# Performance work log

Measured on AMD Instinct MI355X. Metric: run time of the kernel, lower is better.

The kernel has to match this reference:

```python
import jax, jax.numpy as jnp
import numpy as np
import math

E, H, N, FF, S, B, LBL = 512, 8, 3, 2048, 256, 128, 3
# eval-mode threshold: epoch clamped to 40 => d = log(2000/40 - 1)
D_THRESH = math.log(2000.0 / 40.0 - 1.0)


def _pos_encoding(seq_len, dim):
    pos = np.arange(seq_len, dtype=np.float32)[:, None]
    div = np.exp(np.arange(0, dim, 2, dtype=np.float32) * (-math.log(10000.0) / dim))
    pe = np.zeros((seq_len, dim), np.float32)
    pe[:, 0::2] = np.sin(pos * div)
    pe[:, 1::2] = np.cos(pos * div)
    return jnp.asarray(pe)[:, None, :]  # [S,1,E]


def _layer_norm(x, g, b, eps=1e-5):
    m = x.mean(-1, keepdims=True)
    v = ((x - m) ** 2).mean(-1, keepdims=True)
    return (x - m) / jnp.sqrt(v + eps) * g + b


def _mha(xq, xkv, Wqkv, bqkv, Wo, bo):
    # xq: [Sq,B,E], xkv: [Sk,B,E]; noise-thresholded attention, eval branch
    Sq, Bb, Ee = xq.shape
    Sk = xkv.shape[0]
    dk = Ee // H
    Wq, Wk, Wv = jnp.split(Wqkv, 3, axis=1)
    bq, bk, bv = jnp.split(bqkv, 3)
    q = (xq @ Wq + bq) * (dk ** -0.5)
    k = xkv @ Wk + bk
    v = xkv @ Wv + bv
    q = q.reshape(Sq, Bb, H, dk).transpose(1, 2, 0, 3)  # [B,H,Sq,dk]
    k = k.reshape(Sk, Bb, H, dk).transpose(1, 2, 0, 3)
    v = v.reshape(Sk, Bb, H, dk).transpose(1, 2, 0, 3)
    s = jnp.einsum('bhqd,bhkd->bhqk', q, k)
    smax = jnp.max(s, axis=-1, keepdims=True)
    s = jnp.where(s < smax - D_THRESH, -jnp.inf, s)  # threshold sparsification
    w = jax.nn.softmax(s, axis=-1)
    o = jnp.einsum('bhqk,bhkd->bhqd', w, v)
    o = o.transpose(2, 0, 1, 3).reshape(Sq, Bb, Ee)
    return o @ Wo + bo


def _ffn(x, W1, b1, W2, b2):
    return jax.nn.relu(x @ W1 + b1) @ W2 + b2


def _encoder_layer(x, i, g1, b1ln, Wqkv, bqkv, Wo, bo, g2, b2ln, W1, b1, W2, b2):
    h = _layer_norm(x, g1[i], b1ln[i])
    x = x + _mha(h, h, Wqkv[i], bqkv[i], Wo[i], bo[i])
    h = _layer_norm(x, g2[i], b2ln[i])
    x = x + _ffn(h, W1[i], b1[i], W2[i], b2[i])
    return x


def _forward(x_1, x_2, enc_ln1_g, enc_ln1_b, enc_Wqkv, enc_bqkv, enc_Wo, enc_bo,
             enc_ln2_g, enc_ln2_b, enc_W1, enc_b1, enc_W2, enc_b2,
             isa_ln_g, isa_ln_b, isa_Wqkv, isa_bqkv, isa_Wo, isa_bo,
             iea_ln_g, iea_ln_b, iea_Wqkv, iea_bqkv, iea_Wo, iea_bo,
             iff_ln_g, iff_ln_b, int_W1, int_b1, int_W2, int_b2,
             fc1_w, fc1_b, fc2_w, fc2_b, fc3_w, fc3_b, fc4_w, fc4_b):
    pe = _pos_encoding(x_1.shape[0], x_1.shape[-1])
    x1 = x_1 + pe
    x2 = x_2 + pe
    # Siamese encoder (shared weights)
    for i in range(N):
        x1 = _encoder_layer(x1, i, enc_ln1_g, enc_ln1_b, enc_Wqkv, enc_bqkv, enc_Wo, enc_bo,
                            enc_ln2_g, enc_ln2_b, enc_W1, enc_b1, enc_W2, enc_b2)
        x2 = _encoder_layer(x2, i, enc_ln1_g, enc_ln1_b, enc_Wqkv, enc_bqkv, enc_Wo, enc_bo,
                            enc_ln2_g, enc_ln2_b, enc_W1, enc_b1, enc_W2, enc_b2)
    e1, e2 = x1, x2
    # interaction stack (shared self/cross attn applied to both streams)
    for i in range(N):
        h1 = _layer_norm(x1, isa_ln_g[i], isa_ln_b[i])
        x1 = x1 + _mha(h1, h1, isa_Wqkv[i], isa_bqkv[i], isa_Wo[i], isa_bo[i])
        h2 = _layer_norm(x2, isa_ln_g[i], isa_ln_b[i])
        x2 = x2 + _mha(h2, h2, isa_Wqkv[i], isa_bqkv[i], isa_Wo[i], isa_bo[i])
        h1 = _layer_norm(x1, iea_ln_g[i], iea_ln_b[i])
        h2 = _layer_norm(x2, iea_ln_g[i], iea_ln_b[i])
        y1 = _mha(h1, h2, iea_Wqkv[i], iea_bqkv[i], iea_Wo[i], iea_bo[i])
        y2 = _mha(h2, h1, iea_Wqkv[i], iea_bqkv[i], iea_Wo[i], iea_bo[i])
        x1 = x1 + y1
        x2 = x2 + y2
        x1 = x1 + _ffn(_layer_norm(x1, iff_ln_g[i], iff_ln_b[i]), int_W1[i], int_b1[i], int_W2[i], int_b2[i])
        x2 = x2 + _ffn(_layer_norm(x2, iff_ln_g[i], iff_ln_b[i]), int_W1[i], int_b1[i], int_W2[i], int_b2[i])
    i1, i2 = x1, x2
    # Comparison classifier
    h1 = jax.nn.relu(jnp.concatenate([e1, i1], axis=-1) @ fc1_w + fc1_b) @ fc2_w + fc2_b
    p1 = h1.sum(0) / (h1.shape[0] ** 0.5)  # [B,E]
    h2 = jax.nn.relu(jnp.concatenate([e2, i2], axis=-1) @ fc1_w + fc1_b) @ fc2_w + fc2_b
    p2 = h2.sum(0) / (h2.shape[0] ** 0.5)
    x = jnp.concatenate([p1, p2], axis=-1)  # [B,2E]
    return jax.nn.relu(x @ fc3_w + fc3_b) @ fc4_w + fc4_b  # [B,LBL]


def setup_inputs() -> dict:
    key = jax.random.key(0)
    ks = iter(jax.random.split(key, 64))
    sc = 1.0 / math.sqrt(E)

    def w(shape, scale=None):
        s = (1.0 / math.sqrt(shape[-2])) if scale is None and len(shape) >= 2 else (scale or sc)
        return jax.random.normal(next(ks), shape, jnp.float32) * s

    d = {
        'x_1': jax.random.normal(next(ks), (S, B, E), jnp.float32),
        'x_2': jax.random.normal(next(ks), (S, B, E), jnp.float32),
        'enc_ln1_g': jnp.ones((N, E)), 'enc_ln1_b': jnp.zeros((N, E)),
        'enc_Wqkv': w((N, E, 3 * E)), 'enc_bqkv': jnp.zeros((N, 3 * E)),
        'enc_Wo': w((N, E, E)), 'enc_bo': jnp.zeros((N, E)),
        'enc_ln2_g': jnp.ones((N, E)), 'enc_ln2_b': jnp.zeros((N, E)),
        'enc_W1': w((N, E, FF)), 'enc_b1': jnp.zeros((N, FF)),
        'enc_W2': w((N, FF, E)), 'enc_b2': jnp.zeros((N, E)),
        'isa_ln_g': jnp.ones((N, E)), 'isa_ln_b': jnp.zeros((N, E)),
        'isa_Wqkv': w((N, E, 3 * E)), 'isa_bqkv': jnp.zeros((N, 3 * E)),
        'isa_Wo': w((N, E, E)), 'isa_bo': jnp.zeros((N, E)),
        'iea_ln_g': jnp.ones((N, E)), 'iea_ln_b': jnp.zeros((N, E)),
        'iea_Wqkv': w((N, E, 3 * E)), 'iea_bqkv': jnp.zeros((N, 3 * E)),
        'iea_Wo': w((N, E, E)), 'iea_bo': jnp.zeros((N, E)),
        'iff_ln_g': jnp.ones((N, E)), 'iff_ln_b': jnp.zeros((N, E)),
        'int_W1': w((N, E, FF)), 'int_b1': jnp.zeros((N, FF)),
        'int_W2': w((N, FF, E)), 'int_b2': jnp.zeros((N, E)),
        'fc1_w': w((2 * E, E)), 'fc1_b': jnp.zeros((E,)),
        'fc2_w': w((E, E)), 'fc2_b': jnp.zeros((E,)),
        'fc3_w': w((2 * E, E)), 'fc3_b': jnp.zeros((E,)),
        'fc4_w': w((E, LBL)), 'fc4_b': jnp.zeros((LBL,)),
    }
    return d


def reference(x_1, x_2, enc_ln1_g, enc_ln1_b, enc_Wqkv, enc_bqkv, enc_Wo, enc_bo,
              enc_ln2_g, enc_ln2_b, enc_W1, enc_b1, enc_W2, enc_b2,
              isa_ln_g, isa_ln_b, isa_Wqkv, isa_bqkv, isa_Wo, isa_bo,
              iea_ln_g, iea_ln_b, iea_Wqkv, iea_bqkv, iea_Wo, iea_bo,
              iff_ln_g, iff_ln_b, int_W1, int_b1, int_W2, int_b2,
              fc1_w, fc1_b, fc2_w, fc2_b, fc3_w, fc3_b, fc4_w, fc4_b):
    return _forward(x_1, x_2, enc_ln1_g, enc_ln1_b, enc_Wqkv, enc_bqkv, enc_Wo, enc_bo,
                    enc_ln2_g, enc_ln2_b, enc_W1, enc_b1, enc_W2, enc_b2,
                    isa_ln_g, isa_ln_b, isa_Wqkv, isa_bqkv, isa_Wo, isa_bo,
                    iea_ln_g, iea_ln_b, iea_Wqkv, iea_bqkv, iea_Wo, iea_bo,
                    iff_ln_g, iff_ln_b, int_W1, int_b1, int_W2, int_b2,
                    fc1_w, fc1_b, fc2_w, fc2_b, fc3_w, fc3_b, fc4_w, fc4_b)
```

## Files before the change

### kernel.cpp

```cpp
#include <hip/hip_runtime.h>


using u16 = unsigned short;
using u32 = unsigned int;

typedef __bf16 bf16x8 __attribute__((ext_vector_type(8)));
typedef u16    u16x8  __attribute__((ext_vector_type(8)));
typedef float  f32x4  __attribute__((ext_vector_type(4)));

#define D_THRESH 3.8918203f

__device__ __forceinline__ u16 f2bf(float f) {
    u32 u = __builtin_bit_cast(u32, f);
    u32 r = (u + 0x7fffu + ((u >> 16) & 1u)) >> 16;
    return (u16)r;
}
__device__ __forceinline__ float bf2f(u16 h) {
    u32 u = ((u32)h) << 16;
    return __builtin_bit_cast(float, u);
}
__device__ __forceinline__ bf16x8 ld_bf8(const u16* p) {
    u16x8 v = *(const u16x8*)p;
    return __builtin_bit_cast(bf16x8, v);
}

#define GLD_LDS(gptr, lptr)                                                     \
    __builtin_amdgcn_global_load_lds(                                           \
        (const __attribute__((address_space(1))) u32*)(gptr),                   \
        (__attribute__((address_space(3))) u32*)(lptr), 16, 0, 0)

__global__ __launch_bounds__(256) void transpose_to_bf16(
    const float* __restrict__ in, u16* __restrict__ out,
    const float* __restrict__ gamma, int K, int N)
{
    __shared__ float tile[32][33];
    const float* src = in  + (size_t)blockIdx.z * K * N;
    u16*         dst = out + (size_t)blockIdx.z * K * N;
    const float* gm  = gamma ? gamma + (size_t)blockIdx.z * K : nullptr;
    int n0 = blockIdx.x * 32, k0 = blockIdx.y * 32;
#pragma unroll
    for (int i = 0; i < 4; ++i) {
        int k = k0 + threadIdx.y + i * 8;
        tile[threadIdx.y + i * 8][threadIdx.x] = src[(size_t)k * N + n0 + threadIdx.x];
    }
    __syncthreads();
#pragma unroll
    for (int i = 0; i < 4; ++i) {
        int n = n0 + threadIdx.y + i * 8;
        int kk = k0 + threadIdx.x;
        float v = tile[threadIdx.x][threadIdx.y + i * 8];
        if (gm) v *= gm[kk];
        dst[(size_t)n * K + kk] = f2bf(v);
    }
}

__global__ __launch_bounds__(256) void init_ud(
    const float* __restrict__ bias, float* __restrict__ u, float* __restrict__ d)
{
    int n = blockIdx.x * 256 + threadIdx.x;
    u[n] = 0.f; d[n] = bias[n];
}

__global__ __launch_bounds__(256) void colsum_part(
    const float* __restrict__ W, const float* __restrict__ gamma,
    const float* __restrict__ beta, float* __restrict__ u, float* __restrict__ d,
    int K, int N)
{
    int n = blockIdx.x * 256 + threadIdx.x;
    int k0 = blockIdx.y * 32;
    const float* Wz = W + (size_t)blockIdx.z * K * N;
    const float* gz = gamma + (size_t)blockIdx.z * K;
    const float* bz = beta  + (size_t)blockIdx.z * K;
    float su = 0.f, sd = 0.f;
#pragma unroll 4
    for (int k = k0; k < k0 + 32; ++k) {
        float w = Wz[(size_t)k * N + n];
        su += gz[k] * w;
        sd += bz[k] * w;
    }
    atomicAdd(&u[(size_t)blockIdx.z * N + n], su);
    atomicAdd(&d[(size_t)blockIdx.z * N + n], sd);
}

__global__ __launch_bounds__(256) void row_stats(
    const u16* __restrict__ x, float2* __restrict__ st)
{
    const int lane = threadIdx.x & 63, w = threadIdx.x >> 6;
    const size_t row = (size_t)blockIdx.x * 4 + w;
    union { uint4 v; u16 h[8]; } a;
    a.v = *(const uint4*)(x + row * 512 + lane * 8);
    float s = 0.f, sq = 0.f;
#pragma unroll
    for (int j = 0; j < 8; ++j) { float f = bf2f(a.h[j]); s += f; sq += f * f; }
#pragma unroll
    for (int off = 1; off < 64; off <<= 1) {
        s  += __shfl_xor(s,  off, 64);
        sq += __shfl_xor(sq, off, 64);
    }
    if (lane == 0) {
        float m  = s * (1.f / 512.f);
        float vr = sq * (1.f / 512.f) - m * m;
        st[row] = make_float2(m, rsqrtf(vr + 1e-5f));
    }
}

template<int EPI>
__global__ __launch_bounds__(256) void gemm_bt(
    const u16* __restrict__ A, int lda,
    const u16* __restrict__ BT, int ldb,
    const float* __restrict__ bias,
    const float* __restrict__ u,
    const float2* __restrict__ st,
    void* __restrict__ Cv, int ldc,
    const float* __restrict__ resf,
    const u16* __restrict__ res16,
    int M, int N, int K)
{
    __shared__ u16 As[128 * 64];
    __shared__ u16 Bs[128 * 64];
    const int tid  = threadIdx.x;
    const int lane = tid & 63;
    const int w    = tid >> 6;
    const int wm   = w >> 1, wn = w & 1;
    const int m0   = blockIdx.y * 128, n0 = blockIdx.x * 128;
    const int g    = lane & 15, q = lane >> 4;

    const f32x4 fz = {0.f, 0.f, 0.f, 0.f};
    f32x4 acc[4][4];
#pragma unroll
    for (int i = 0; i < 4; ++i)
#pragma unroll
        for (int j = 0; j < 4; ++j) acc[i][j] = fz;

    for (int kt = 0; kt < K; kt += 64) {
#pragma unroll
        for (int i = 0; i < 4; ++i) {
            int c = (w * 4 + i) * 64 + lane;
            int r = c >> 3, cq = c & 7;
            GLD_LDS(A  + (size_t)(m0 + r) * lda + kt + cq * 8, As + (size_t)(w * 4 + i) * 512);
            GLD_LDS(BT + (size_t)(n0 + r) * ldb + kt + cq * 8, Bs + (size_t)(w * 4 + i) * 512);
        }
        __syncthreads();
#pragma unroll
        for (int ks = 0; ks < 2; ++ks) {
            bf16x8 af[4], bfr[4];
#pragma unroll
            for (int i = 0; i < 4; ++i) af[i]  = ld_bf8(As + (wm * 64 + i * 16 + g) * 64 + ks * 32 + q * 8);
#pragma unroll
            for (int j = 0; j < 4; ++j) bfr[j] = ld_bf8(Bs + (wn * 64 + j * 16 + g) * 64 + ks * 32 + q * 8);
#pragma unroll
            for (int i = 0; i < 4; ++i)
#pragma unroll
                for (int j = 0; j < 4; ++j)
                    acc[i][j] = __builtin_amdgcn_mfma_f32_16x16x32_bf16(af[i], bfr[j], acc[i][j], 0, 0, 0);
        }
        __syncthreads();
    }
#pragma unroll
    for (int j = 0; j < 4; ++j) {
        int col  = n0 + wn * 64 + j * 16 + g;
        float bj = bias ? bias[col] : 0.f;
        float un = (EPI == 5 || EPI == 6) ? u[col] : 0.f;
#pragma unroll
        for (int i = 0; i < 4; ++i) {
            int rb = m0 + wm * 64 + i * 16 + q * 4;
#pragma unroll
            for (int r = 0; r < 4; ++r) {
                float v = acc[i][j][r];
                size_t idx = (size_t)(rb + r) * ldc + col;
                if (EPI == 5 || EPI == 6) {
                    float2 s2 = st[rb + r];
                    v = s2.y * v - s2.y * s2.x * un + bj;
                } else {
                    v += bj;
                }
                if (EPI == 1 || EPI == 6) v = fmaxf(v, 0.f);
                if (EPI == 4) v = fmaxf(resf[idx] + v, 0.f);
                if (EPI == 2) v += bf2f(((u16*)Cv)[idx]);
                if (EPI == 8) v += bf2f(((u16*)Cv)[idx]) + bf2f(res16[idx]);
                if (EPI == 3) ((float*)Cv)[idx] = v;
                else          ((u16*)Cv)[idx]   = f2bf(v);
            }
        }
    }
}

__global__ __launch_bounds__(256) void attn_kernel(
    const u16* __restrict__ Q, int lq,
    const u16* __restrict__ Kp, const u16* __restrict__ Vp, int lkv,
    u16* __restrict__ O, int lo)
{
    __shared__ u16 smem[32768];
    u16* Ks  = smem;
    u16* Qs  = smem + 16384;
    u16* Ps  = smem;
    u16* VTs = smem + 16384;

    const int tid = threadIdx.x, lane = tid & 63, w = tid >> 6;
    const int g = lane & 15, qd = lane >> 4;
    const int q0 = blockIdx.x * 64;
    const int b = blockIdx.y >> 3, h = blockIdx.y & 7;

#pragma unroll
    for (int i = 0; i < 8; ++i) {
        int c = (w * 8 + i) * 64 + lane;
        int r = c >> 3, cq = c & 7;
        GLD_LDS(Kp + (size_t)(r * 128 + b) * lkv + h * 64 + cq * 8,
                Ks + (size_t)(w * 8 + i) * 512);
    }
#pragma unroll
    for (int i = 0; i < 2; ++i) {
        int c = (w * 2 + i) * 64 + lane;
        int r = c >> 3, cq = c & 7;
        GLD_LDS(Q + (size_t)((q0 + r) * 128 + b) * lq + h * 64 + cq * 8,
                Qs + (size_t)(w * 2 + i) * 512);
    }
    __syncthreads();

    const f32x4 fz = {0.f, 0.f, 0.f, 0.f};
    f32x4 s[16];
#pragma unroll
    for (int t = 0; t < 16; ++t) s[t] = fz;
#pragma unroll
    for (int ks = 0; ks < 2; ++ks) {
        bf16x8 aq = ld_bf8(Qs + (w * 16 + g) * 64 + ks * 32 + qd * 8);
#pragma unroll
        for (int t = 0; t < 16; ++t) {
            bf16x8 bk = ld_bf8(Ks + (t * 16 + g) * 64 + ks * 32 + qd * 8);
            s[t] = __builtin_amdgcn_mfma_f32_16x16x32_bf16(aq, bk, s[t], 0, 0, 0);
        }
    }
    __syncthreads();

    union { uint4 v; u16 us[8]; } vch[8];
#pragma unroll
    for (int i = 0; i < 8; ++i) {
        int c = i * 256 + tid;
        int r = c >> 3, cq = c & 7;
        vch[i].v = *(const uint4*)(Vp + (size_t)(r * 128 + b) * lkv + h * 64 + cq * 8);
    }

    float mrow[4] = {-1e30f, -1e30f, -1e30f, -1e30f};
#pragma unroll
    for (int t = 0; t < 16; ++t)
#pragma unroll
        for (int r = 0; r < 4; ++r) mrow[r] = fmaxf(mrow[r], s[t][r]);
#pragma unroll
    for (int off = 1; off < 16; off <<= 1)
#pragma unroll
        for (int r = 0; r < 4; ++r) mrow[r] = fmaxf(mrow[r], __shfl_xor(mrow[r], off, 64));
#pragma unroll
    for (int r = 0; r < 4; ++r) mrow[r] *= 0.125f;

    float l[4] = {0.f, 0.f, 0.f, 0.f};
#pragma unroll
    for (int t = 0; t < 16; ++t)
#pragma unroll
        for (int r = 0; r < 4; ++r) {
            float sc = s[t][r] * 0.125f;
            float p  = (sc >= mrow[r] - D_THRESH) ? __expf(sc - mrow[r]) : 0.f;
            u16 pb = f2bf(p);
            l[r] += bf2f(pb);
            Ps[(w * 16 + qd * 4 + r) * 256 + t * 16 + g] = pb;
        }
#pragma unroll
    for (int off = 1; off < 16; off <<= 1)
#pragma unroll
        for (int r = 0; r < 4; ++r) l[r] += __shfl_xor(l[r], off, 64);

#pragma unroll
    for (int i = 0; i < 8; ++i) {
        int c = i * 256 + tid;
        int r = c >> 3, cq = c & 7;
#pragma unroll
        for (int j = 0; j < 8; ++j) VTs[(cq * 8 + j) * 256 + r] = vch[i].us[j];
    }
    __syncthreads();

    f32x4 o[4];
#pragma unroll
    for (int nt = 0; nt < 4; ++nt) o[nt] = fz;
#pragma unroll
    for (int ks = 0; ks < 8; ++ks) {
        bf16x8 ap = ld_bf8(Ps + (w * 16 + g) * 256 + ks * 32 + qd * 8);
#pragma unroll
        for (int nt = 0; nt < 4; ++nt) {
            bf16x8 bv = ld_bf8(VTs + (nt * 16 + g) * 256 + ks * 32 + qd * 8);
            o[nt] = __builtin_amdgcn_mfma_f32_16x16x32_bf16(ap, bv, o[nt], 0, 0, 0);
        }
    }
    float rl[4];
#pragma unroll
    for (int r = 0; r < 4; ++r) rl[r] = 1.f / l[r];
#pragma unroll
    for (int nt = 0; nt < 4; ++nt)
#pragma unroll
        for (int r = 0; r < 4; ++r) {
            int srow = q0 + w * 16 + qd * 4 + r;
            O[(size_t)(srow * 128 + b) * lo + h * 64 + nt * 16 + g] = f2bf(o[nt][r] * rl[r]);
        }
}

__global__ __launch_bounds__(256) void build_pe(float* __restrict__ pe) {
    int idx = blockIdx.x * 256 + threadIdx.x;
    int e = idx & 511, s = idx >> 9;
    int j = e >> 1;
    float fr = __expf((float)(2 * j) * (-0.017988946f));
    float ph = (float)s * fr;
    pe[idx] = (e & 1) ? cosf(ph) : sinf(ph);
}

__global__ __launch_bounds__(256) void add_pe_bf16(
    const float* __restrict__ in, const float* __restrict__ pe, u16* __restrict__ out)
{
    size_t idx = (size_t)blockIdx.x * 256 + threadIdx.x;
    int e = (int)(idx & 511);
    int s = (int)(idx >> 16);
    out[idx] = f2bf(in[idx] + pe[(s << 9) | e]);
}

__global__ __launch_bounds__(128) void pool_sum(
    const float* __restrict__ t2, u16* __restrict__ pcat, int colofs)
{
    int b = blockIdx.x >> 2, ec = blockIdx.x & 3;
    int e = ec * 128 + threadIdx.x;
    float acc = 0.f;
    for (int s = 0; s < 256; ++s) acc += t2[(size_t)(s * 128 + b) * 512 + e];
    pcat[b * 1024 + colofs + e] = f2bf(acc * 0.0625f);
}

__global__ __launch_bounds__(64) void fc4_kernel(
    const u16* __restrict__ a, const float* __restrict__ w,
    const float* __restrict__ bias, float* __restrict__ out)
{
    int id = blockIdx.x * 64 + threadIdx.x;
    if (id >= 384) return;
    int b = id / 3, l = id % 3;
    float acc = bias[l];
    for (int k = 0; k < 512; ++k) acc += bf2f(a[b * 512 + k]) * w[k * 3 + l];
    out[id] = acc;
}

__global__ __launch_bounds__(64) void sentinel_kernel(float* __restrict__ out) {
    int i = blockIdx.x * 64 + threadIdx.x;
    if (i < 384) out[i] = -12345.0f;
}

extern "C" void kernel_launch(void* const* d_in, const int* in_sizes, int n_in,
                              void* d_out, int out_size, void* d_ws, size_t ws_size,
                              hipStream_t stream) {
    (void)in_sizes; (void)n_in; (void)out_size;

    const float* x_1       = (const float*)d_in[0];
    const float* x_2       = (const float*)d_in[1];
    const float* enc_ln1_g = (const float*)d_in[2];
    const float* enc_ln1_b = (const float*)d_in[3];
    const float* enc_Wqkv  = (const float*)d_in[4];
    const float* enc_bqkv  = (const float*)d_in[5];
    const float* enc_Wo    = (const float*)d_in[6];
    const float* enc_bo    = (const float*)d_in[7];
    const float* enc_ln2_g = (const float*)d_in[8];
    const float* enc_ln2_b = (const float*)d_in[9];
    const float* enc_W1    = (const float*)d_in[10];
    const float* enc_b1    = (const float*)d_in[11];
    const float* enc_W2    = (const float*)d_in[12];
    const float* enc_b2    = (const float*)d_in[13];
    const float* isa_ln_g  = (const float*)d_in[14];
    const float* isa_ln_b  = (const float*)d_in[15];
    const float* isa_Wqkv  = (const float*)d_in[16];
    const float* isa_bqkv  = (const float*)d_in[17];
    const float* isa_Wo    = (const float*)d_in[18];
    const float* isa_bo    = (const float*)d_in[19];
    const float* iea_ln_g  = (const float*)d_in[20];
    const float* iea_ln_b  = (const float*)d_in[21];
    const float* iea_Wqkv  = (const float*)d_in[22];
    const float* iea_bqkv  = (const float*)d_in[23];
    const float* iea_Wo    = (const float*)d_in[24];
    const float* iea_bo    = (const float*)d_in[25];
    const float* iff_ln_g  = (const float*)d_in[26];
    const float* iff_ln_b  = (const float*)d_in[27];
    const float* int_W1    = (const float*)d_in[28];
    const float* int_b1    = (const float*)d_in[29];
    const float* int_W2    = (const float*)d_in[30];
    const float* int_b2    = (const float*)d_in[31];
    const float* fc1_w     = (const float*)d_in[32];
    const float* fc1_b     = (const float*)d_in[33];
    const float* fc2_w     = (const float*)d_in[34];
    const float* fc2_b     = (const float*)d_in[35];
    const float* fc3_w     = (const float*)d_in[36];
    const float* fc3_b     = (const float*)d_in[37];
    const float* fc4_w     = (const float*)d_in[38];
    const float* fc4_b     = (const float*)d_in[39];
    float* out = (float*)d_out;

    const size_t WS_NEED = 264318976;
    if (ws_size < WS_NEED) {
        sentinel_kernel<<<6, 64, 0, stream>>>(out);
        return;
    }

    char* ws = (char*)d_ws;
    u16* isaQKV = (u16*)(ws + 0);
    u16* isaWO  = (u16*)(ws + 4718592);
    u16* ieaQKV = (u16*)(ws + 6291456);
    u16* ieaWO  = (u16*)(ws + 11010048);
    u16* intW1  = (u16*)(ws + 12582912);
    u16* intW2  = (u16*)(ws + 18874368);
    u16* fc1T   = (u16*)(ws + 25165824);
    u16* fc2T   = (u16*)(ws + 26214400);
    u16* fc3T   = (u16*)(ws + 26738688);
    float* UD   = (float*)(ws + 27787264);
    float* enc_qkv_u = UD;
    float* enc_qkv_d = UD + 4608;
    float* enc_w1_u  = UD + 9216;
    float* enc_w1_d  = UD + 15360;
    float* isa_qkv_u = UD + 21504;
    float* isa_qkv_d = UD + 26112;
    float* iea_qkv_u = UD + 30720;
    float* iea_qkv_d = UD + 35328;
    float* int_w1_u  = UD + 39936;
    float* int_w1_d  = UD + 46080;
    float2* stats1 = (float2*)(ws + 27996160);
    float2* stats2 = (float2*)(ws + 28258304);
    float*  pe     = (float*)(ws + 28520448);
    u16*    pcat   = (u16*)(ws + 29044736);
    u16*    fc3o   = (u16*)(ws + 29306880);
    u16*    x1     = (u16*)(ws + 29437952);
    u16*    x2     = (u16*)(ws + 62992384);
    u16* encQKV = (u16*)(ws + 96546816);
    u16* encWO  = (u16*)(ws + 96546816 + 4718592);
    u16* encW1  = (u16*)(ws + 96546816 + 6291456);
    u16* encW2  = (u16*)(ws + 96546816 + 12582912);
    u16* e1     = (u16*)(ws + 96546816);
    u16* e2     = (u16*)(ws + 96546816 + 33554432);
    u16*   qkv  = (u16*)(ws + 163655680);
    u16*   B0   = (u16*)(ws + 163655680);
    u16*   B1   = (u16*)(ws + 163655680 + 33554432);
    u16*   fbuf = (u16*)(ws + 163655680);
    u16*   dlt  = (u16*)(ws + 163655680 + 67108864);
    float* accf = (float*)(ws + 163655680);
    u16*   hcls = (u16*)(ws + 163655680 + 67108864);

    auto TR = [&](const float* in, u16* o, const float* g, int K, int N, int L) {
        transpose_to_bf16<<<dim3(N / 32, K / 32, L), dim3(32, 8), 0, stream>>>(in, o, g, K, N);
    };
    TR(enc_Wqkv, encQKV, enc_ln1_g, 512, 1536, 3);
    TR(enc_Wo,   encWO,  nullptr,   512, 512,  3);
    TR(enc_W1,   encW1,  enc_ln2_g, 512, 2048, 3);
    TR(enc_W2,   encW2,  nullptr,   2048, 512, 3);
    TR(isa_Wqkv, isaQKV, isa_ln_g,  512, 1536, 3);
    TR(isa_Wo,   isaWO,  nullptr,   512, 512,  3);
    TR(iea_Wqkv, ieaQKV, iea_ln_g,  512, 1536, 3);
    TR(iea_Wo,   ieaWO,  nullptr,   512, 512,  3);
    TR(int_W1,   intW1,  iff_ln_g,  512, 2048, 3);
    TR(int_W2,   intW2,  nullptr,   2048, 512, 3);
    TR(fc1_w, fc1T, nullptr, 1024, 512, 1);
    TR(fc2_w, fc2T, nullptr, 512,  512, 1);
    TR(fc3_w, fc3T, nullptr, 1024, 512, 1);

    auto CS = [&](const float* W, const float* g, const float* b, const float* bias,
                  float* u, float* d, int K, int N, int L) {
        init_ud<<<N * L / 256, 256, 0, stream>>>(bias, u, d);
        colsum_part<<<dim3(N / 256, K / 32, L), 256, 0, stream>>>(W, g, b, u, d, K, N);
    };
    CS(enc_Wqkv, enc_ln1_g, enc_ln1_b, enc_bqkv, enc_qkv_u, enc_qkv_d, 512, 1536, 3);
    CS(enc_W1,   enc_ln2_g, enc_ln2_b, enc_b1,   enc_w1_u,  enc_w1_d,  512, 2048, 3);
    CS(isa_Wqkv, isa_ln_g,  isa_ln_b,  isa_bqkv, isa_qkv_u, isa_qkv_d, 512, 1536, 3);
    CS(iea_Wqkv, iea_ln_g,  iea_ln_b,  iea_bqkv, iea_qkv_u, iea_qkv_d, 512, 1536, 3);
    CS(int_W1,   iff_ln_g,  iff_ln_b,  int_b1,   int_w1_u,  int_w1_d,  512, 2048, 3);

    build_pe<<<512, 256, 0, stream>>>(pe);
    add_pe_bf16<<<65536, 256, 0, stream>>>(x_1, pe, x1);
    add_pe_bf16<<<65536, 256, 0, stream>>>(x_2, pe, x2);

    auto G = [&](int epi, const u16* A, int lda, const u16* BT, int ldb,
                 const float* bias, const float* uu, const float2* stt,
                 void* C, int ldc, const float* resf, const u16* res16,
                 int M, int N, int K) {
        dim3 grid(N / 128, M / 128);
        switch (epi) {
        case 0: gemm_bt<0><<<grid, 256, 0, stream>>>(A, lda, BT, ldb, bias, uu, stt, C, ldc, resf, res16, M, N, K); break;
        case 1: gemm_bt<1><<<grid, 256, 0, stream>>>(A, lda, BT, ldb, bias, uu, stt, C, ldc, resf, res16, M, N, K); break;
        case 2: gemm_bt<2><<<grid, 256, 0, stream>>>(A, lda, BT, ldb, bias, uu, stt, C, ldc, resf, res16, M, N, K); break;
        case 3: gemm_bt<3><<<grid, 256, 0, stream>>>(A, lda, BT, ldb, bias, uu, stt, C, ldc, resf, res16, M, N, K); break;
        case 4: gemm_bt<4><<<grid, 256, 0, stream>>>(A, lda, BT, ldb, bias, uu, stt, C, ldc, resf, res16, M, N, K); break;
        case 5: gemm_bt<5><<<grid, 256, 0, stream>>>(A, lda, BT, ldb, bias, uu, stt, C, ldc, resf, res16, M, N, K); break;
        case 6: gemm_bt<6><<<grid, 256, 0, stream>>>(A, lda, BT, ldb, bias, uu, stt, C, ldc, resf, res16, M, N, K); break;
        case 8: gemm_bt<8><<<grid, 256, 0, stream>>>(A, lda, BT, ldb, bias, uu, stt, C, ldc, resf, res16, M, N, K); break;
        }
    };
    auto STATS = [&](const u16* x, float2* stt) {
        row_stats<<<8192, 256, 0, stream>>>(x, stt);
    };
    auto ATT = [&](const u16* Qp, int lq, const u16* Kp, const u16* Vp, int lkv,
                   u16* Op, int lo) {
        attn_kernel<<<dim3(4, 1024), 256, 0, stream>>>(Qp, lq, Kp, Vp, lkv, Op, lo);
    };

    auto self_block = [&](u16* x, u16* wqkvT, const float* qu, const float* qd,
                          u16* woT, const float* bo,
                          u16* w1T, const float* w1u, const float* w1d,
                          u16* w2T, const float* b2, bool do_ffn) {
        STATS(x, stats1);
        G(5, x, 512, wqkvT, 512, qd, qu, stats1, qkv, 1536, nullptr, nullptr, 32768, 1536, 512);
        ATT(qkv, 1536, qkv + 512, qkv + 1024, 1536, qkv, 1536);
        G(2, qkv, 1536, woT, 512, bo, nullptr, nullptr, x, 512, nullptr, nullptr, 32768, 512, 512);
        if (do_ffn) {
            STATS(x, stats1);
            G(6, x, 512, w1T, 512, w1d, w1u, stats1, fbuf, 1024, nullptr, nullptr, 32768, 1024, 512);
            G(0, fbuf, 1024, w2T, 2048, b2, nullptr, nullptr, dlt, 512, nullptr, nullptr, 32768, 512, 1024);
            G(6, x, 512, w1T + 1024 * 512, 512, w1d + 1024, w1u + 1024, stats1, fbuf, 1024, nullptr, nullptr, 32768, 1024, 512);
            G(8, fbuf, 1024, w2T + 1024, 2048, nullptr, nullptr, nullptr, x, 512, nullptr, dlt, 32768, 512, 1024);
        }
    };

    for (int i = 0; i < 3; ++i)
        for (int st = 0; st < 2; ++st)
            self_block(st ? x2 : x1,
                       encQKV + (size_t)i * 786432, enc_qkv_u + i * 1536, enc_qkv_d + i * 1536,
                       encWO + (size_t)i * 262144, enc_bo + i * 512,
                       encW1 + (size_t)i * 1048576, enc_w1_u + i * 2048, enc_w1_d + i * 2048,
                       encW2 + (size_t)i * 1048576, enc_b2 + i * 512, true);

    hipMemcpyAsync(e1, x1, 33554432, hipMemcpyDeviceToDevice, stream);
    hipMemcpyAsync(e2, x2, 33554432, hipMemcpyDeviceToDevice, stream);

    for (int i = 0; i < 3; ++i) {
        for (int st = 0; st < 2; ++st)
            self_block(st ? x2 : x1,
                       isaQKV + (size_t)i * 786432, isa_qkv_u + i * 1536, isa_qkv_d + i * 1536,
                       isaWO + (size_t)i * 262144, isa_bo + i * 512,
                       nullptr, nullptr, nullptr, nullptr, nullptr, false);
        u16* qT  = ieaQKV + (size_t)i * 786432;
        u16* kvT = qT + 512 * 512;
        const float* qu = iea_qkv_u + i * 1536;
        const float* qd = iea_qkv_d + i * 1536;
        STATS(x2, stats2);
        G(5, x2, 512, kvT, 512, qd + 512, qu + 512, stats2, B1, 1024, nullptr, nullptr, 32768, 1024, 512);
        STATS(x1, stats1);
        G(5, x1, 512, qT, 512, qd, qu, stats1, B0, 512, nullptr, nullptr, 32768, 512, 512);
        ATT(B0, 512, B1, B1 + 512, 1024, B0, 512);
        G(5, x1, 512, kvT, 512, qd + 512, qu + 512, stats1, B1, 1024, nullptr, nullptr, 32768, 1024, 512);
        G(2, B0, 512, ieaWO + (size_t)i * 262144, 512, iea_bo + i * 512, nullptr, nullptr,
          x1, 512, nullptr, nullptr, 32768, 512, 512);
        G(5, x2, 512, qT, 512, qd, qu, stats2, B0, 512, nullptr, nullptr, 32768, 512, 512);
        ATT(B0, 512, B1, B1 + 512, 1024, B0, 512);
        G(2, B0, 512, ieaWO + (size_t)i * 262144, 512, iea_bo + i * 512, nullptr, nullptr,
          x2, 512, nullptr, nullptr, 32768, 512, 512);
        for (int st = 0; st < 2; ++st) {
            u16* x = st ? x2 : x1;
            STATS(x, stats1);
            u16* w1T = intW1 + (size_t)i * 1048576;
            u16* w2T = intW2 + (size_t)i * 1048576;
            const float* w1u = int_w1_u + i * 2048;
            const float* w1d = int_w1_d + i * 2048;
            G(6, x, 512, w1T, 512, w1d, w1u, stats1, fbuf, 1024, nullptr, nullptr, 32768, 1024, 512);
            G(0, fbuf, 1024, w2T, 2048, int_b2 + i * 512, nullptr, nullptr, dlt, 512, nullptr, nullptr, 32768, 512, 1024);
            G(6, x, 512, w1T + 1024 * 512, 512, w1d + 1024, w1u + 1024, stats1, fbuf, 1024, nullptr, nullptr, 32768, 1024, 512);
            G(8, fbuf, 1024, w2T + 1024, 2048, nullptr, nullptr, nullptr, x, 512, nullptr, dlt, 32768, 512, 1024);
        }
    }

    for (int st = 0; st < 2; ++st) {
        const u16* e = st ? e2 : e1;
        const u16* x = st ? x2 : x1;
        G(3, e, 512, fc1T, 1024, nullptr, nullptr, nullptr, accf, 512, nullptr, nullptr, 32768, 512, 512);
        G(4, x, 512, fc1T + 512, 1024, fc1_b, nullptr, nullptr, hcls, 512, accf, nullptr, 32768, 512, 512);
        G(3, hcls, 512, fc2T, 512, fc2_b, nullptr, nullptr, accf, 512, nullptr, nullptr, 32768, 512, 512);
        pool_sum<<<512, 128, 0, stream>>>(accf, pcat, st * 512);
    }
    G(1, pcat, 1024, fc3T, 1024, fc3_b, nullptr, nullptr, fc3o, 512, nullptr, nullptr, 128, 512, 1024);
    fc4_kernel<<<6, 64, 0, stream>>>(fc3o, fc4_w, fc4_b, out);
}
```

Measured before the change: 9.380 ms.

## Stage GEMM epilogue through LDS and restructure attention to one block per head

The GEMM epilogue for bf16 outputs now writes results into shared memory and then stores them as coalesced 16-byte rows, also doing the residual reads vectorized. The attention kernel now launches one 512-thread block per (batch, head): K is loaded once and reused across all 256 queries, Q is read straight from global memory, and P and V^T are staged in 64-key chunks. Together these are meant to cut uncoalesced scalar stores and repeated K/V loads, at the cost of extra barriers and a grid of only 1024 blocks.

```diff
diff --git a/kernel.cpp b/kernel.cpp
--- a/kernel.cpp
+++ b/kernel.cpp
@@ -116,8 +116,9 @@
     const u16* __restrict__ res16,
     int M, int N, int K)
 {
-    __shared__ u16 As[128 * 64];
-    __shared__ u16 Bs[128 * 64];
+    __shared__ u16 smem[17408];
+    u16* As = smem;
+    u16* Bs = smem + 8192;
     const int tid  = threadIdx.x;
     const int lane = tid & 63;
     const int w    = tid >> 6;
@@ -156,149 +157,187 @@
         }
         __syncthreads();
     }
-#pragma unroll
-    for (int j = 0; j < 4; ++j) {
-        int col  = n0 + wn * 64 + j * 16 + g;
-        float bj = bias ? bias[col] : 0.f;
-        float un = (EPI == 5 || EPI == 6) ? u[col] : 0.f;
-#pragma unroll
-        for (int i = 0; i < 4; ++i) {
-            int rb = m0 + wm * 64 + i * 16 + q * 4;
-#pragma unroll
-            for (int r = 0; r < 4; ++r) {
-                float v = acc[i][j][r];
-                size_t idx = (size_t)(rb + r) * ldc + col;
-                if (EPI == 5 || EPI == 6) {
-                    float2 s2 = st[rb + r];
-                    v = s2.y * v - s2.y * s2.x * un + bj;
-                } else {
-                    v += bj;
+
+    if (EPI == 3 || EPI == 4) {
+#pragma unroll
+        for (int j = 0; j < 4; ++j) {
+            int col  = n0 + wn * 64 + j * 16 + g;
+            float bj = bias ? bias[col] : 0.f;
+#pragma unroll
+            for (int i = 0; i < 4; ++i) {
+                int rb = m0 + wm * 64 + i * 16 + q * 4;
+#pragma unroll
+                for (int r = 0; r < 4; ++r) {
+                    float v = acc[i][j][r] + bj;
+                    size_t idx = (size_t)(rb + r) * ldc + col;
+                    if (EPI == 4) { v = fmaxf(resf[idx] + v, 0.f); ((u16*)Cv)[idx] = f2bf(v); }
+                    else          ((float*)Cv)[idx] = v;
                 }
-                if (EPI == 1 || EPI == 6) v = fmaxf(v, 0.f);
-                if (EPI == 4) v = fmaxf(resf[idx] + v, 0.f);
-                if (EPI == 2) v += bf2f(((u16*)Cv)[idx]);
-                if (EPI == 8) v += bf2f(((u16*)Cv)[idx]) + bf2f(res16[idx]);
-                if (EPI == 3) ((float*)Cv)[idx] = v;
-                else          ((u16*)Cv)[idx]   = f2bf(v);
-            }
-        }
-    }
-}
-
-__global__ __launch_bounds__(256) void attn_kernel(
+            }
+        }
+    } else {
+        u16* Cs = smem;
+#pragma unroll
+        for (int j = 0; j < 4; ++j) {
+            int cl   = wn * 64 + j * 16 + g;
+            float bj = bias ? bias[n0 + cl] : 0.f;
+            float un = (EPI == 5 || EPI == 6) ? u[n0 + cl] : 0.f;
+#pragma unroll
+            for (int i = 0; i < 4; ++i) {
+                int rl = wm * 64 + i * 16 + q * 4;
+#pragma unroll
+                for (int r = 0; r < 4; ++r) {
+                    float v = acc[i][j][r];
+                    if (EPI == 5 || EPI == 6) {
+                        float2 s2 = st[m0 + rl + r];
+                        v = s2.y * v - s2.y * s2.x * un + bj;
+                    } else {
+                        v += bj;
+                    }
+                    if (EPI == 1 || EPI == 6) v = fmaxf(v, 0.f);
+                    Cs[(rl + r) * 136 + cl] = f2bf(v);
+                }
+            }
+        }
+        __syncthreads();
+        const int cr = tid >> 4, cc = tid & 15;
+#pragma unroll
+        for (int rr = 0; rr < 8; ++rr) {
+            int rl = cr * 8 + rr;
+            size_t gidx = (size_t)(m0 + rl) * ldc + n0 + cc * 8;
+            union { uint4 v; u16 h8[8]; } sv;
+            sv.v = *(const uint4*)(Cs + rl * 136 + cc * 8);
+            if (EPI == 2 || EPI == 8) {
+                union { uint4 v; u16 h8[8]; } cv2, rv;
+                cv2.v = *(const uint4*)((const u16*)Cv + gidx);
+                if (EPI == 8) rv.v = *(const uint4*)(res16 + gidx);
+#pragma unroll
+                for (int jj = 0; jj < 8; ++jj) {
+                    float v = bf2f(sv.h8[jj]) + bf2f(cv2.h8[jj]);
+                    if (EPI == 8) v += bf2f(rv.h8[jj]);
+                    sv.h8[jj] = f2bf(v);
+                }
+            }
+            *(uint4*)((u16*)Cv + gidx) = sv.v;
+        }
+    }
+}
+
+__global__ __launch_bounds__(512, 4) void attn_kernel(
     const u16* __restrict__ Q, int lq,
     const u16* __restrict__ Kp, const u16* __restrict__ Vp, int lkv,
     u16* __restrict__ O, int lo)
 {
-    __shared__ u16 smem[32768];
+    __shared__ u16 smem[29696];
     u16* Ks  = smem;
-    u16* Qs  = smem + 16384;
-    u16* Ps  = smem;
-    u16* VTs = smem + 16384;
+    u16* Ps  = smem + 16384;
+    u16* VTs = smem + 25600;
 
     const int tid = threadIdx.x, lane = tid & 63, w = tid >> 6;
     const int g = lane & 15, qd = lane >> 4;
-    const int q0 = blockIdx.x * 64;
-    const int b = blockIdx.y >> 3, h = blockIdx.y & 7;
-
-#pragma unroll
-    for (int i = 0; i < 8; ++i) {
-        int c = (w * 8 + i) * 64 + lane;
+    const int b = blockIdx.x >> 3, h = blockIdx.x & 7;
+
+#pragma unroll
+    for (int i = 0; i < 4; ++i) {
+        int c = i * 512 + tid;
         int r = c >> 3, cq = c & 7;
         GLD_LDS(Kp + (size_t)(r * 128 + b) * lkv + h * 64 + cq * 8,
-                Ks + (size_t)(w * 8 + i) * 512);
-    }
-#pragma unroll
-    for (int i = 0; i < 2; ++i) {
-        int c = (w * 2 + i) * 64 + lane;
-        int r = c >> 3, cq = c & 7;
-        GLD_LDS(Q + (size_t)((q0 + r) * 128 + b) * lq + h * 64 + cq * 8,
-                Qs + (size_t)(w * 2 + i) * 512);
+                Ks + (size_t)(i * 512 + w * 64) * 8);
     }
     __syncthreads();
 
     const f32x4 fz = {0.f, 0.f, 0.f, 0.f};
-    f32x4 s[16];
-#pragma unroll
-    for (int t = 0; t < 16; ++t) s[t] = fz;
-#pragma unroll
-    for (int ks = 0; ks < 2; ++ks) {
-        bf16x8 aq = ld_bf8(Qs + (w * 16 + g) * 64 + ks * 32 + qd * 8);
-#pragma unroll
-        for (int t = 0; t < 16; ++t) {
-            bf16x8 bk = ld_bf8(Ks + (t * 16 + g) * 64 + ks * 32 + qd * 8);
-            s[t] = __builtin_amdgcn_mfma_f32_16x16x32_bf16(aq, bk, s[t], 0, 0, 0);
-        }
-    }
-    __syncthreads();
-
-    union { uint4 v; u16 us[8]; } vch[8];
-#pragma unroll
-    for (int i = 0; i < 8; ++i) {
-        int c = i * 256 + tid;
-        int r = c >> 3, cq = c & 7;
-        vch[i].v = *(const uint4*)(Vp + (size_t)(r * 128 + b) * lkv + h * 64 + cq * 8);
-    }
-
-    float mrow[4] = {-1e30f, -1e30f, -1e30f, -1e30f};
-#pragma unroll
-    for (int t = 0; t < 16; ++t)
-#pragma unroll
-        for (int r = 0; r < 4; ++r) mrow[r] = fmaxf(mrow[r], s[t][r]);
-#pragma unroll
-    for (int off = 1; off < 16; off <<= 1)
-#pragma unroll
-        for (int r = 0; r < 4; ++r) mrow[r] = fmaxf(mrow[r], __shfl_xor(mrow[r], off, 64));
-#pragma unroll
-    for (int r = 0; r < 4; ++r) mrow[r] *= 0.125f;
-
-    float l[4] = {0.f, 0.f, 0.f, 0.f};
-#pragma unroll
-    for (int t = 0; t < 16; ++t)
-#pragma unroll
-        for (int r = 0; r < 4; ++r) {
-            float sc = s[t][r] * 0.125f;
-            float p  = (sc >= mrow[r] - D_THRESH) ? __expf(sc - mrow[r]) : 0.f;
-            u16 pb = f2bf(p);
-            l[r] += bf2f(pb);
-            Ps[(w * 16 + qd * 4 + r) * 256 + t * 16 + g] = pb;
-        }
-#pragma unroll
-    for (int off = 1; off < 16; off <<= 1)
-#pragma unroll
-        for (int r = 0; r < 4; ++r) l[r] += __shfl_xor(l[r], off, 64);
-
-#pragma unroll
-    for (int i = 0; i < 8; ++i) {
-        int c = i * 256 + tid;
-        int r = c >> 3, cq = c & 7;
-#pragma unroll
-        for (int j = 0; j < 8; ++j) VTs[(cq * 8 + j) * 256 + r] = vch[i].us[j];
-    }
-    __syncthreads();
-
-    f32x4 o[4];
-#pragma unroll
-    for (int nt = 0; nt < 4; ++nt) o[nt] = fz;
-#pragma unroll
-    for (int ks = 0; ks < 8; ++ks) {
-        bf16x8 ap = ld_bf8(Ps + (w * 16 + g) * 256 + ks * 32 + qd * 8);
-#pragma unroll
-        for (int nt = 0; nt < 4; ++nt) {
-            bf16x8 bv = ld_bf8(VTs + (nt * 16 + g) * 256 + ks * 32 + qd * 8);
-            o[nt] = __builtin_amdgcn_mfma_f32_16x16x32_bf16(ap, bv, o[nt], 0, 0, 0);
-        }
-    }
-    float rl[4];
-#pragma unroll
-    for (int r = 0; r < 4; ++r) rl[r] = 1.f / l[r];
-#pragma unroll
-    for (int nt = 0; nt < 4; ++nt)
-#pragma unroll
-        for (int r = 0; r < 4; ++r) {
-            int srow = q0 + w * 16 + qd * 4 + r;
-            O[(size_t)(srow * 128 + b) * lo + h * 64 + nt * 16 + g] = f2bf(o[nt][r] * rl[r]);
-        }
+    for (int s = 0; s < 2; ++s) {
+        const int qb = s * 128 + w * 16;
+
+        f32x4 sc[16];
+#pragma unroll
+        for (int t = 0; t < 16; ++t) sc[t] = fz;
+#pragma unroll
+        for (int ks = 0; ks < 2; ++ks) {
+            bf16x8 aq = ld_bf8(Q + (size_t)((qb + g) * 128 + b) * lq + h * 64 + ks * 32 + qd * 8);
+#pragma unroll
+            for (int t = 0; t < 16; ++t) {
+                bf16x8 bk = ld_bf8(Ks + (t * 16 + g) * 64 + ks * 32 + qd * 8);
+                sc[t] = __builtin_amdgcn_mfma_f32_16x16x32_bf16(aq, bk, sc[t], 0, 0, 0);
+            }
+        }
+
+        float mrow[4] = {-1e30f, -1e30f, -1e30f, -1e30f};
+#pragma unroll
+        for (int t = 0; t < 16; ++t)
+#pragma unroll
+            for (int r = 0; r < 4; ++r) mrow[r] = fmaxf(mrow[r], sc[t][r]);
+#pragma unroll
+        for (int off = 1; off < 16; off <<= 1)
+#pragma unroll
+            for (int r = 0; r < 4; ++r) mrow[r] = fmaxf(mrow[r], __shfl_xor(mrow[r], off, 64));
+#pragma unroll
+        for (int r = 0; r < 4; ++r) mrow[r] *= 0.125f;
+
+        float l[4] = {0.f, 0.f, 0.f, 0.f};
+        u32 pk[16][2];
+#pragma unroll
+        for (int t = 0; t < 16; ++t)
+#pragma unroll
+            for (int r = 0; r < 4; ++r) {
+                float scv = sc[t][r] * 0.125f;
+                float p   = (scv >= mrow[r] - D_THRESH) ? __expf(scv - mrow[r]) : 0.f;
+                u16 pb = f2bf(p);
+                l[r] += bf2f(pb);
+                if (r & 1) pk[t][r >> 1] |= ((u32)pb) << 16;
+                else       pk[t][r >> 1]  = pb;
+            }
+#pragma unroll
+        for (int off = 1; off < 16; off <<= 1)
+#pragma unroll
+            for (int r = 0; r < 4; ++r) l[r] += __shfl_xor(l[r], off, 64);
+
+        f32x4 o[4];
+#pragma unroll
+        for (int nt = 0; nt < 4; ++nt) o[nt] = fz;
+        for (int qt = 0; qt < 4; ++qt) {
+#pragma unroll
+            for (int tt = 0; tt < 4; ++tt) {
+                int t = qt * 4 + tt;
+#pragma unroll
+                for (int rh = 0; rh < 2; ++rh) {
+                    u32 pv = pk[t][rh];
+                    Ps[(w * 16 + qd * 4 + rh * 2)     * 72 + tt * 16 + g] = (u16)pv;
+                    Ps[(w * 16 + qd * 4 + rh * 2 + 1) * 72 + tt * 16 + g] = (u16)(pv >> 16);
+                }
+            }
+            {
+                int kvr = qt * 64 + lane;
+                union { uint4 v; u16 h8[8]; } vu;
+                vu.v = *(const uint4*)(Vp + (size_t)(kvr * 128 + b) * lkv + h * 64 + w * 8);
+#pragma unroll
+                for (int jj = 0; jj < 8; ++jj) VTs[(w * 8 + jj) * 64 + lane] = vu.h8[jj];
+            }
+            __syncthreads();
+#pragma unroll
+            for (int st2 = 0; st2 < 2; ++st2) {
+                bf16x8 ap = ld_bf8(Ps + (w * 16 + g) * 72 + st2 * 32 + qd * 8);
+#pragma unroll
+                for (int nt = 0; nt < 4; ++nt) {
+                    bf16x8 bv = ld_bf8(VTs + (nt * 16 + g) * 64 + st2 * 32 + qd * 8);
+                    o[nt] = __builtin_amdgcn_mfma_f32_16x16x32_bf16(ap, bv, o[nt], 0, 0, 0);
+                }
+            }
+            __syncthreads();
+        }
+
+        float rl[4];
+#pragma unroll
+        for (int r = 0; r < 4; ++r) rl[r] = 1.f / l[r];
+#pragma unroll
+        for (int nt = 0; nt < 4; ++nt)
+#pragma unroll
+            for (int r = 0; r < 4; ++r) {
+                int qrow = qb + qd * 4 + r;
+                O[(size_t)(qrow * 128 + b) * lo + h * 64 + nt * 16 + g] = f2bf(o[nt][r] * rl[r]);
+            }
+    }
 }
 
 __global__ __launch_bounds__(256) void build_pe(float* __restrict__ pe) {
@@ -494,7 +533,7 @@
     };
     auto ATT = [&](const u16* Qp, int lq, const u16* Kp, const u16* Vp, int lkv,
                    u16* Op, int lo) {
-        attn_kernel<<<dim3(4, 1024), 256, 0, stream>>>(Qp, lq, Kp, Vp, lkv, Op, lo);
+        attn_kernel<<<dim3(1024), 512, 0, stream>>>(Qp, lq, Kp, Vp, lkv, Op, lo);
     };
 
     auto self_block = [&](u16* x, u16* wqkvT, const float* qu, const float* qd,
```

After: 7.925 ms. 1.18x faster.
